# Kernel tuning notes

Measured on AMD Instinct MI355X. Metric: run time of the kernel, lower is better.

## Reference

```python
import jax, jax.numpy as jnp
import numpy as np

B, S, D, H = 2, 2048, 1024, 16
DK = D // H

def setup_inputs() -> dict:
    key = jax.random.key(0)
    ks = jax.random.split(key, 12)
    scale = 1.0 / np.sqrt(D)
    inp = {
        'q': jax.random.normal(ks[0], (B, S, D), jnp.float32),
        'k': jax.random.normal(ks[1], (B, S, D), jnp.float32),
        'v': jax.random.normal(ks[2], (B, S, D), jnp.float32),
        # causal mask: 1 where attending is allowed (j <= i), 0 for future tokens
        'mask': jnp.tril(jnp.ones((S, S), jnp.int32))[None, None, :, :],
        'wq': jax.random.normal(ks[3], (D, D), jnp.float32) * scale,
        'bq': jnp.zeros((D,), jnp.float32),
        'wk': jax.random.normal(ks[4], (D, D), jnp.float32) * scale,
        'bk': jnp.zeros((D,), jnp.float32),
        'wv': jax.random.normal(ks[5], (D, D), jnp.float32) * scale,
        'bv': jnp.zeros((D,), jnp.float32),
        'wo': jax.random.normal(ks[6], (D, D), jnp.float32) * scale,
        'bo': jnp.zeros((D,), jnp.float32),
    }
    return inp


def reference(q, k, v, mask, wq, bq, wk, bk, wv, bv, wo, bo):
    def split_heads(x):
        # [B,S,D] -> [B,H,S,DK]
        return x.reshape(B, S, H, DK).transpose(0, 2, 1, 3)

    query = split_heads(q @ wq + bq)
    key_ = split_heads(k @ wk + bk)
    value = split_heads(v @ wv + bv)

    # [B,H,S,S] attention scores
    scores = jnp.einsum('bhqd,bhkd->bhqk', query, key_) / jnp.sqrt(
        jnp.asarray(DK, jnp.float32))
    scores = jnp.where(mask == 0, jnp.asarray(-1e9, scores.dtype), scores)
    attn = jax.nn.softmax(scores, axis=-1)  # dropout p=0.0 (eval mode)

    x = jnp.einsum('bhqk,bhkd->bhqd', attn, value)  # [B,H,S,DK]
    x = x.transpose(0, 2, 1, 3).reshape(B, S, D)
    return x @ wo + bo
```

## Files before the change

kernel.cpp:

```cpp
#include <hip/hip_runtime.h>
#include <hip/hip_bf16.h>

#define BATCH 2
#define SEQ   2048
#define DMODEL 1024
#define NHEAD 16
#define DK    64
#define MTOK  (BATCH * SEQ)

typedef __attribute__((ext_vector_type(8))) short bf16x8;
typedef __attribute__((ext_vector_type(4))) float f32x4;

__device__ __forceinline__ unsigned short f2bf(float x) {
    unsigned u = __float_as_uint(x);
    u = (u + 0x7FFFu + ((u >> 16) & 1u)) >> 16;
    return (unsigned short)u;
}

__device__ __forceinline__ void store_out(float* p, float v)          { *p = v; }
__device__ __forceinline__ void store_out(unsigned short* p, float v) { *p = f2bf(v); }

__device__ __forceinline__ void g2lds16(const void* g, void* l) {
    __builtin_amdgcn_global_load_lds(
        (const __attribute__((address_space(1))) void*)g,
        (__attribute__((address_space(3))) void*)l, 16, 0, 0);
}

__global__ __launch_bounds__(256) void cvt3_bf16_kernel(
    const float* __restrict__ s0, const float* __restrict__ s1,
    const float* __restrict__ s2,
    unsigned short* __restrict__ d0, unsigned short* __restrict__ d1,
    unsigned short* __restrict__ d2, int n)
{
    const float* src; unsigned short* dst;
    switch (blockIdx.z) {
        case 0:  src = s0; dst = d0; break;
        case 1:  src = s1; dst = d1; break;
        default: src = s2; dst = d2; break;
    }
    int i = (blockIdx.x * 256 + threadIdx.x) * 8;
    if (i >= n) return;
    float4 a = *(const float4*)(src + i);
    float4 b = *(const float4*)(src + i + 4);
    union { unsigned short s[8]; uint4 u; } o;
    o.s[0] = f2bf(a.x); o.s[1] = f2bf(a.y); o.s[2] = f2bf(a.z); o.s[3] = f2bf(a.w);
    o.s[4] = f2bf(b.x); o.s[5] = f2bf(b.y); o.s[6] = f2bf(b.z); o.s[7] = f2bf(b.w);
    *(uint4*)(dst + i) = o.u;
}

__global__ __launch_bounds__(256) void wtrans_kernel(
    const float* __restrict__ w0, const float* __restrict__ w1,
    const float* __restrict__ w2, const float* __restrict__ w3,
    unsigned short* __restrict__ t0, unsigned short* __restrict__ t1,
    unsigned short* __restrict__ t2, unsigned short* __restrict__ t3)
{
    __shared__ float tile[32][33];
    const float* W; unsigned short* T;
    switch (blockIdx.z) {
        case 0:  W = w0; T = t0; break;
        case 1:  W = w1; T = t1; break;
        case 2:  W = w2; T = t2; break;
        default: W = w3; T = t3; break;
    }
    const int n0 = blockIdx.x * 32, k0 = blockIdx.y * 32;
    const int t  = threadIdx.x;
    const int r  = t >> 3;
    const int c4 = (t & 7) * 4;

    float4 v = *(const float4*)&W[(size_t)(k0 + r) * DMODEL + n0 + c4];
    tile[r][c4 + 0] = v.x; tile[r][c4 + 1] = v.y;
    tile[r][c4 + 2] = v.z; tile[r][c4 + 3] = v.w;
    __syncthreads();

    union { unsigned short s[4]; uint2 u; } o;
#pragma unroll
    for (int u = 0; u < 4; ++u) o.s[u] = f2bf(tile[c4 + u][r]);
    *(uint2*)&T[(size_t)(n0 + r) * DMODEL + k0 + c4] = o.u;
}

struct GemmP {
    const unsigned short* A;
    const unsigned short* Bt;
    const float* bias;
    void* C;
    int N, K, ctShift, biasByRow;
    float scale;
};
struct Gemm3 { GemmP p[3]; };

template <typename OutT, int NTILE>
__global__ __launch_bounds__(256) void gemm_lds_kernel(Gemm3 g)
{
    __shared__ unsigned short sA[16 * 512];
    __shared__ unsigned short sB[4 * NTILE * 512];

    const GemmP p = g.p[blockIdx.z];
    const unsigned short* __restrict__ A  = p.A;
    const unsigned short* __restrict__ Bt = p.Bt;
    OutT* __restrict__ C = (OutT*)p.C;
    const int K = p.K, N = p.N;

    const int bid = blockIdx.x;
    const int bx = bid & ((1 << p.ctShift) - 1);
    const int by = bid >> p.ctShift;
    const int row0 = by * 128;
    const int col0 = bx * (NTILE * 32);

    const int t    = threadIdx.x;
    const int w    = t >> 6;
    const int lane = t & 63;
    const int ln   = lane & 15;
    const int qg   = lane >> 4;
    const int wm   = w >> 1;
    const int wn   = w & 1;

    const int PW = 4 + NTILE;
    const unsigned short* sp[PW];
    unsigned short* lp[PW];
#pragma unroll
    for (int i = 0; i < PW; ++i) {
        const int s = w * PW + i;
        if (s < 16) {
            const int mtg = s >> 1, kc = s & 1;
            sp[i] = A + (size_t)(row0 + mtg * 16 + ln) * K + kc * 32 + qg * 8;
            lp[i] = &sA[s * 512];
        } else {
            const int bi = s - 16;
            const int ntg = bi >> 1, kc = bi & 1;
            sp[i] = Bt + (size_t)(col0 + ntg * 16 + ln) * K + kc * 32 + qg * 8;
            lp[i] = &sB[bi * 512];
        }
    }

    f32x4 acc[4][NTILE];
#pragma unroll
    for (int mt = 0; mt < 4; ++mt)
#pragma unroll
        for (int nt = 0; nt < NTILE; ++nt) acc[mt][nt] = (f32x4){0.f, 0.f, 0.f, 0.f};

    for (int kt = 0; kt < K / 64; ++kt) {
        __syncthreads();
        const int koff = kt * 64;
#pragma unroll
        for (int i = 0; i < PW; ++i)
            g2lds16(sp[i] + koff, lp[i]);
        __syncthreads();

#pragma unroll
        for (int kc = 0; kc < 2; ++kc) {
            bf16x8 aF[4], bF[NTILE];
#pragma unroll
            for (int mt = 0; mt < 4; ++mt)
                aF[mt] = *(const bf16x8*)&sA[(((wm * 4 + mt) * 2) + kc) * 512 + lane * 8];
#pragma unroll
            for (int nt = 0; nt < NTILE; ++nt)
                bF[nt] = *(const bf16x8*)&sB[(((wn * NTILE + nt) * 2) + kc) * 512 + lane * 8];
#pragma unroll
            for (int mt = 0; mt < 4; ++mt)
#pragma unroll
                for (int nt = 0; nt < NTILE; ++nt)
                    acc[mt][nt] = __builtin_amdgcn_mfma_f32_16x16x32_bf16(
                        aF[mt], bF[nt], acc[mt][nt], 0, 0, 0);
        }
    }

    float bcol[NTILE], brow[4][4];
    if (!p.biasByRow) {
#pragma unroll
        for (int nt = 0; nt < NTILE; ++nt)
            bcol[nt] = p.bias[col0 + wn * NTILE * 16 + nt * 16 + ln];
    } else {
#pragma unroll
        for (int mt = 0; mt < 4; ++mt)
#pragma unroll
            for (int r = 0; r < 4; ++r)
                brow[mt][r] = p.bias[row0 + wm * 64 + mt * 16 + qg * 4 + r];
    }

#pragma unroll
    for (int mt = 0; mt < 4; ++mt)
#pragma unroll
        for (int nt = 0; nt < NTILE; ++nt)
#pragma unroll
            for (int r = 0; r < 4; ++r) {
                int row = row0 + wm * 64 + mt * 16 + qg * 4 + r;
                int col = col0 + wn * NTILE * 16 + nt * 16 + ln;
                float bb = p.biasByRow ? brow[mt][r] : bcol[nt];
                store_out(&C[(size_t)row * N + col], (acc[mt][nt][r] + bb) * p.scale);
            }
}

#define BR 64
#define BC 64
#define PSTR 72

__global__ __launch_bounds__(256) void attn_mfma_kernel(
    const unsigned short* __restrict__ Qg, const unsigned short* __restrict__ Kg,
    const unsigned short* __restrict__ VT, unsigned short* __restrict__ O)
{
    __shared__ unsigned short sK[2][8 * 512];
    __shared__ unsigned short sV[2][8 * 512];
    __shared__ unsigned short sQ[8 * 512];
    __shared__ unsigned short sP[BR * PSTR];

    const int t    = threadIdx.x;
    const int w    = t >> 6;
    const int lane = t & 63;
    const int ln   = lane & 15;
    const int qg   = lane >> 4;

    const int id  = blockIdx.x;
    const int bh  = id & 31;
    const int qt  = (SEQ / BR - 1) - (id >> 5);
    const int b   = bh >> 4;
    const int h   = bh & 15;
    const int qi0 = qt * BR;

    const size_t rowbase = (size_t)b * SEQ;
    const size_t colbase = (size_t)h * DK;

#pragma unroll
    for (int i = 0; i < 2; ++i) {
        const int s = w * 2 + i;
        const int nt = s >> 1, kc = s & 1;
        g2lds16(Qg + (rowbase + qi0 + w * 16 + ln) * DMODEL + colbase + i * 32 + qg * 8,
                &sQ[s * 512]);
        g2lds16(Kg + (rowbase + nt * 16 + ln) * DMODEL + colbase + kc * 32 + qg * 8,
                &sK[0][s * 512]);
        g2lds16(VT + (size_t)(colbase + nt * 16 + ln) * MTOK + rowbase + kc * 32 + qg * 8,
                &sV[0][s * 512]);
    }
    __syncthreads();

    bf16x8 aq[2];
#pragma unroll
    for (int kc = 0; kc < 2; ++kc)
        aq[kc] = *(const bf16x8*)&sQ[(w * 2 + kc) * 512 + lane * 8];

    const short one_bf = (short)0x3F80;
    const bf16x8 bone = (bf16x8){one_bf, one_bf, one_bf, one_bf,
                                 one_bf, one_bf, one_bf, one_bf};

    f32x4 ofrag[4];
#pragma unroll
    for (int nt = 0; nt < 4; ++nt) ofrag[nt] = (f32x4){0.f, 0.f, 0.f, 0.f};
    f32x4 osum = (f32x4){0.f, 0.f, 0.f, 0.f};
    float m_r[4];
#pragma unroll
    for (int r = 0; r < 4; ++r) m_r[r] = -3.0e38f;

    const int ntiles = qt + 1;
    for (int jt = 0; jt < ntiles; ++jt) {
        const int cur = jt & 1;

        if (jt + 1 < ntiles) {
            const int j1 = (jt + 1) * BC;
            const int nb = cur ^ 1;
#pragma unroll
            for (int i = 0; i < 2; ++i) {
                const int s = w * 2 + i;
                const int nt = s >> 1, kc = s & 1;
                g2lds16(Kg + (rowbase + j1 + nt * 16 + ln) * DMODEL + colbase + kc * 32 + qg * 8,
                        &sK[nb][s * 512]);
                g2lds16(VT + (size_t)(colbase + nt * 16 + ln) * MTOK + rowbase + j1 + kc * 32 + qg * 8,
                        &sV[nb][s * 512]);
            }
        }

        f32x4 sf[4];
#pragma unroll
        for (int nt = 0; nt < 4; ++nt) {
            f32x4 a2 = (f32x4){0.f, 0.f, 0.f, 0.f};
#pragma unroll
            for (int kc = 0; kc < 2; ++kc) {
                bf16x8 bk = *(const bf16x8*)&sK[cur][(nt * 2 + kc) * 512 + lane * 8];
                a2 = __builtin_amdgcn_mfma_f32_16x16x32_bf16(aq[kc], bk, a2, 0, 0, 0);
            }
            sf[nt] = a2;
        }

        if (jt == ntiles - 1) {
#pragma unroll
            for (int nt = 0; nt < 4; ++nt)
#pragma unroll
                for (int r = 0; r < 4; ++r) {
                    int qrow = w * 16 + qg * 4 + r;
                    int col  = nt * 16 + ln;
                    if (col > qrow) sf[nt][r] = -1.0e30f;
                }
        }

        float rmax[4];
#pragma unroll
        for (int r = 0; r < 4; ++r)
            rmax[r] = fmaxf(fmaxf(sf[0][r], sf[1][r]), fmaxf(sf[2][r], sf[3][r]));
#pragma unroll
        for (int off = 8; off >= 1; off >>= 1)
#pragma unroll
            for (int r = 0; r < 4; ++r)
                rmax[r] = fmaxf(rmax[r], __shfl_xor(rmax[r], off));

        float alpha[4];
#pragma unroll
        for (int r = 0; r < 4; ++r) {
            float mn = fmaxf(m_r[r], rmax[r]);
            alpha[r] = exp2f(m_r[r] - mn);
            m_r[r] = mn;
        }

#pragma unroll
        for (int nt = 0; nt < 4; ++nt)
#pragma unroll
            for (int r = 0; r < 4; ++r) {
                float pv = exp2f(sf[nt][r] - m_r[r]);
                int row = w * 16 + qg * 4 + r;
                int col = (nt * 16 + ln) ^ (((w * 4 + qg) & 7) * 8);
                sP[row * PSTR + col] = f2bf(pv);
            }

#pragma unroll
        for (int nt = 0; nt < 4; ++nt)
#pragma unroll
            for (int r = 0; r < 4; ++r) ofrag[nt][r] *= alpha[r];
#pragma unroll
        for (int r = 0; r < 4; ++r) osum[r] *= alpha[r];

        bf16x8 apf[2];
#pragma unroll
        for (int kc = 0; kc < 2; ++kc) {
            int row = w * 16 + ln;
            int col = (kc * 32 + qg * 8) ^ ((((row >> 2) & 7)) * 8);
            apf[kc] = *(const bf16x8*)&sP[row * PSTR + col];
        }

#pragma unroll
        for (int kc = 0; kc < 2; ++kc)
            osum = __builtin_amdgcn_mfma_f32_16x16x32_bf16(apf[kc], bone, osum, 0, 0, 0);
#pragma unroll
        for (int nt = 0; nt < 4; ++nt) {
#pragma unroll
            for (int kc = 0; kc < 2; ++kc) {
                bf16x8 bv = *(const bf16x8*)&sV[cur][(nt * 2 + kc) * 512 + lane * 8];
                ofrag[nt] = __builtin_amdgcn_mfma_f32_16x16x32_bf16(apf[kc], bv, ofrag[nt], 0, 0, 0);
            }
        }

        __syncthreads();
    }

    float inv[4];
#pragma unroll
    for (int r = 0; r < 4; ++r) inv[r] = 1.0f / osum[r];
#pragma unroll
    for (int nt = 0; nt < 4; ++nt)
#pragma unroll
        for (int r = 0; r < 4; ++r) {
            int gq = qi0 + w * 16 + qg * 4 + r;
            O[(rowbase + gq) * DMODEL + colbase + nt * 16 + ln] =
                f2bf(ofrag[nt][r] * inv[r]);
        }
}

extern "C" void kernel_launch(void* const* d_in, const int* in_sizes, int n_in,
                              void* d_out, int out_size, void* d_ws, size_t ws_size,
                              hipStream_t stream)
{
    const float* q  = (const float*)d_in[0];
    const float* k  = (const float*)d_in[1];
    const float* v  = (const float*)d_in[2];
    const float* wq = (const float*)d_in[4];
    const float* bq = (const float*)d_in[5];
    const float* wk = (const float*)d_in[6];
    const float* bk = (const float*)d_in[7];
    const float* wv = (const float*)d_in[8];
    const float* bv = (const float*)d_in[9];
    const float* wo = (const float*)d_in[10];
    const float* bo = (const float*)d_in[11];
    float* out = (float*)d_out;

    const size_t mat  = (size_t)MTOK * DMODEL;
    const size_t wmat = (size_t)DMODEL * DMODEL;
    unsigned short* Abq = (unsigned short*)d_ws;
    unsigned short* Abk = Abq + mat;
    unsigned short* Abv = Abk + mat;
    unsigned short* WtQ = Abv + mat;
    unsigned short* WtK = WtQ + wmat;
    unsigned short* WtV = WtK + wmat;
    unsigned short* WtO = WtV + wmat;
    unsigned short* Qb  = WtO + wmat;
    unsigned short* Kb  = Qb + mat;
    unsigned short* VT  = Kb + mat;
    unsigned short* CTX = VT + mat;

    cvt3_bf16_kernel<<<dim3((unsigned)(mat / 2048), 1, 3), 256, 0, stream>>>(
        q, k, v, Abq, Abk, Abv, (int)mat);
    wtrans_kernel<<<dim3(32, 32, 4), 256, 0, stream>>>(wq, wk, wv, wo, WtQ, WtK, WtV, WtO);

    const float qscale = 0.125f * 1.44269504088896f;
    Gemm3 g;
    g.p[0] = (GemmP){Abq, WtQ, bq, (void*)Qb, DMODEL, DMODEL, 3, 0, qscale};
    g.p[1] = (GemmP){Abk, WtK, bk, (void*)Kb, DMODEL, DMODEL, 3, 0, 1.0f};
    g.p[2] = (GemmP){WtV, Abv, bv, (void*)VT, MTOK,   DMODEL, 5, 1, 1.0f};
    gemm_lds_kernel<unsigned short, 4><<<dim3(256, 1, 3), 256, 0, stream>>>(g);

    attn_mfma_kernel<<<BATCH * NHEAD * (SEQ / BR), 256, 0, stream>>>(Qb, Kb, VT, CTX);

    Gemm3 go;
    go.p[0] = (GemmP){CTX, WtO, bo, (void*)out, DMODEL, DMODEL, 4, 0, 1.0f};
    go.p[1] = go.p[0];
    go.p[2] = go.p[0];
    gemm_lds_kernel<float, 2><<<dim3(512, 1, 1), 256, 0, stream>>>(go);
}
```

Baseline: 272.6 us.

## Fuse fp32-to-bf16 activation conversion into GEMM and process two query tiles per attention block

Drops the separate activation conversion kernel: the projection GEMM now loads fp32 A or B tiles straight into LDS and packs them to bf16 when reading fragments. This removes a full write and re-read of the three activation matrices, at the cost of twice the LDS footprint and extra conversion work in the GEMM inner loop. The attention kernel now gives each block two 64-row query tiles, so each K/V tile is reused across both, and it halves the grid with a 2-blocks-per-CU launch bound. The added accumulator state may raise register pressure.

```diff
diff --git a/kernel.cpp b/kernel.cpp
--- a/kernel.cpp
+++ b/kernel.cpp
@@ -26,26 +26,13 @@
         (__attribute__((address_space(3))) void*)l, 16, 0, 0);
 }
 
-__global__ __launch_bounds__(256) void cvt3_bf16_kernel(
-    const float* __restrict__ s0, const float* __restrict__ s1,
-    const float* __restrict__ s2,
-    unsigned short* __restrict__ d0, unsigned short* __restrict__ d1,
-    unsigned short* __restrict__ d2, int n)
-{
-    const float* src; unsigned short* dst;
-    switch (blockIdx.z) {
-        case 0:  src = s0; dst = d0; break;
-        case 1:  src = s1; dst = d1; break;
-        default: src = s2; dst = d2; break;
-    }
-    int i = (blockIdx.x * 256 + threadIdx.x) * 8;
-    if (i >= n) return;
-    float4 a = *(const float4*)(src + i);
-    float4 b = *(const float4*)(src + i + 4);
-    union { unsigned short s[8]; uint4 u; } o;
-    o.s[0] = f2bf(a.x); o.s[1] = f2bf(a.y); o.s[2] = f2bf(a.z); o.s[3] = f2bf(a.w);
-    o.s[4] = f2bf(b.x); o.s[5] = f2bf(b.y); o.s[6] = f2bf(b.z); o.s[7] = f2bf(b.w);
-    *(uint4*)(dst + i) = o.u;
+__device__ __forceinline__ bf16x8 pack8(f32x4 lo, f32x4 hi) {
+    union { bf16x8 v; __hip_bfloat162 h[4]; } u;
+    u.h[0] = __float22bfloat162_rn(float2{lo[0], lo[1]});
+    u.h[1] = __float22bfloat162_rn(float2{lo[2], lo[3]});
+    u.h[2] = __float22bfloat162_rn(float2{hi[0], hi[1]});
+    u.h[3] = __float22bfloat162_rn(float2{hi[2], hi[3]});
+    return u.v;
 }
 
 __global__ __launch_bounds__(256) void wtrans_kernel(
@@ -79,26 +66,24 @@
 }
 
 struct GemmP {
-    const unsigned short* A;
-    const unsigned short* Bt;
+    const void* A;
+    const void* Bt;
     const float* bias;
     void* C;
-    int N, K, ctShift, biasByRow;
+    int N, K, ctShift, biasByRow, aF32, bF32;
     float scale;
 };
 struct Gemm3 { GemmP p[3]; };
 
-template <typename OutT, int NTILE>
+template <typename OutT, int NTILE, int TOTB>
 __global__ __launch_bounds__(256) void gemm_lds_kernel(Gemm3 g)
 {
-    __shared__ unsigned short sA[16 * 512];
-    __shared__ unsigned short sB[4 * NTILE * 512];
+    __shared__ unsigned char smem[TOTB * 1024];
 
     const GemmP p = g.p[blockIdx.z];
-    const unsigned short* __restrict__ A  = p.A;
-    const unsigned short* __restrict__ Bt = p.Bt;
     OutT* __restrict__ C = (OutT*)p.C;
     const int K = p.K, N = p.N;
+    const int nA = p.aF32 ? 32 : 16;
 
     const int bid = blockIdx.x;
     const int bx = bid & ((1 << p.ctShift) - 1);
@@ -114,23 +99,40 @@
     const int wm   = w >> 1;
     const int wn   = w & 1;
 
-    const int PW = 4 + NTILE;
-    const unsigned short* sp[PW];
-    unsigned short* lp[PW];
+    const int PW = TOTB / 4;
+    const unsigned char* sp[PW];
+    int bstep[PW];
 #pragma unroll
     for (int i = 0; i < PW; ++i) {
         const int s = w * PW + i;
-        if (s < 16) {
-            const int mtg = s >> 1, kc = s & 1;
-            sp[i] = A + (size_t)(row0 + mtg * 16 + ln) * K + kc * 32 + qg * 8;
-            lp[i] = &sA[s * 512];
+        if (s < nA) {
+            if (p.aF32) {
+                const int mtg = s >> 2, kc = (s >> 1) & 1, half = s & 1;
+                sp[i] = (const unsigned char*)p.A +
+                        ((size_t)(row0 + mtg * 16 + ln) * K + kc * 32 + qg * 8 + half * 4) * 4;
+                bstep[i] = 256;
+            } else {
+                const int mtg = s >> 1, kc = s & 1;
+                sp[i] = (const unsigned char*)p.A +
+                        ((size_t)(row0 + mtg * 16 + ln) * K + kc * 32 + qg * 8) * 2;
+                bstep[i] = 128;
+            }
         } else {
-            const int bi = s - 16;
-            const int ntg = bi >> 1, kc = bi & 1;
-            sp[i] = Bt + (size_t)(col0 + ntg * 16 + ln) * K + kc * 32 + qg * 8;
-            lp[i] = &sB[bi * 512];
-        }
-    }
+            const int bi = s - nA;
+            if (p.bF32) {
+                const int ntg = bi >> 2, kc = (bi >> 1) & 1, half = bi & 1;
+                sp[i] = (const unsigned char*)p.Bt +
+                        ((size_t)(col0 + ntg * 16 + ln) * K + kc * 32 + qg * 8 + half * 4) * 4;
+                bstep[i] = 256;
+            } else {
+                const int ntg = bi >> 1, kc = bi & 1;
+                sp[i] = (const unsigned char*)p.Bt +
+                        ((size_t)(col0 + ntg * 16 + ln) * K + kc * 32 + qg * 8) * 2;
+                bstep[i] = 128;
+            }
+        }
+    }
+    unsigned char* const sB = smem + nA * 1024;
 
     f32x4 acc[4][NTILE];
 #pragma unroll
@@ -140,21 +142,38 @@
 
     for (int kt = 0; kt < K / 64; ++kt) {
         __syncthreads();
-        const int koff = kt * 64;
-#pragma unroll
-        for (int i = 0; i < PW; ++i)
-            g2lds16(sp[i] + koff, lp[i]);
+#pragma unroll
+        for (int i = 0; i < PW; ++i) {
+            g2lds16(sp[i], smem + (w * PW + i) * 1024);
+            sp[i] += bstep[i];
+        }
         __syncthreads();
 
 #pragma unroll
         for (int kc = 0; kc < 2; ++kc) {
             bf16x8 aF[4], bF[NTILE];
 #pragma unroll
-            for (int mt = 0; mt < 4; ++mt)
-                aF[mt] = *(const bf16x8*)&sA[(((wm * 4 + mt) * 2) + kc) * 512 + lane * 8];
-#pragma unroll
-            for (int nt = 0; nt < NTILE; ++nt)
-                bF[nt] = *(const bf16x8*)&sB[(((wn * NTILE + nt) * 2) + kc) * 512 + lane * 8];
+            for (int mt = 0; mt < 4; ++mt) {
+                const int fb = ((wm * 4 + mt) * 2) + kc;
+                if (p.aF32) {
+                    f32x4 lo = *(const f32x4*)(smem + (fb * 2 + 0) * 1024 + lane * 16);
+                    f32x4 hi = *(const f32x4*)(smem + (fb * 2 + 1) * 1024 + lane * 16);
+                    aF[mt] = pack8(lo, hi);
+                } else {
+                    aF[mt] = *(const bf16x8*)(smem + fb * 1024 + lane * 16);
+                }
+            }
+#pragma unroll
+            for (int nt = 0; nt < NTILE; ++nt) {
+                const int fb = ((wn * NTILE + nt) * 2) + kc;
+                if (p.bF32) {
+                    f32x4 lo = *(const f32x4*)(sB + (fb * 2 + 0) * 1024 + lane * 16);
+                    f32x4 hi = *(const f32x4*)(sB + (fb * 2 + 1) * 1024 + lane * 16);
+                    bF[nt] = pack8(lo, hi);
+                } else {
+                    bF[nt] = *(const bf16x8*)(sB + fb * 1024 + lane * 16);
+                }
+            }
 #pragma unroll
             for (int mt = 0; mt < 4; ++mt)
 #pragma unroll
@@ -190,18 +209,16 @@
             }
 }
 
-#define BR 64
-#define BC 64
 #define PSTR 72
 
-__global__ __launch_bounds__(256) void attn_mfma_kernel(
+__global__ __launch_bounds__(256, 2) void attn_mfma_kernel(
     const unsigned short* __restrict__ Qg, const unsigned short* __restrict__ Kg,
     const unsigned short* __restrict__ VT, unsigned short* __restrict__ O)
 {
+    __shared__ unsigned short sQ[16 * 512];
     __shared__ unsigned short sK[2][8 * 512];
     __shared__ unsigned short sV[2][8 * 512];
-    __shared__ unsigned short sQ[8 * 512];
-    __shared__ unsigned short sP[BR * PSTR];
+    __shared__ unsigned short sP[64 * PSTR];
 
     const int t    = threadIdx.x;
     const int w    = t >> 6;
@@ -211,20 +228,27 @@
 
     const int id  = blockIdx.x;
     const int bh  = id & 31;
-    const int qt  = (SEQ / BR - 1) - (id >> 5);
+    const int Pp  = 15 - (id >> 5);
     const int b   = bh >> 4;
     const int h   = bh & 15;
-    const int qi0 = qt * BR;
+    const int qbase = Pp * 128;
 
     const size_t rowbase = (size_t)b * SEQ;
     const size_t colbase = (size_t)h * DK;
 
+#pragma unroll
+    for (int st = 0; st < 2; ++st)
+#pragma unroll
+        for (int i = 0; i < 2; ++i) {
+            const int sidx = (st * 4 + w) * 2 + i;
+            g2lds16(Qg + (rowbase + qbase + st * 64 + w * 16 + ln) * DMODEL
+                        + colbase + i * 32 + qg * 8,
+                    &sQ[sidx * 512]);
+        }
 #pragma unroll
     for (int i = 0; i < 2; ++i) {
         const int s = w * 2 + i;
         const int nt = s >> 1, kc = s & 1;
-        g2lds16(Qg + (rowbase + qi0 + w * 16 + ln) * DMODEL + colbase + i * 32 + qg * 8,
-                &sQ[s * 512]);
         g2lds16(Kg + (rowbase + nt * 16 + ln) * DMODEL + colbase + kc * 32 + qg * 8,
                 &sK[0][s * 512]);
         g2lds16(VT + (size_t)(colbase + nt * 16 + ln) * MTOK + rowbase + kc * 32 + qg * 8,
@@ -232,29 +256,35 @@
     }
     __syncthreads();
 
-    bf16x8 aq[2];
-#pragma unroll
-    for (int kc = 0; kc < 2; ++kc)
-        aq[kc] = *(const bf16x8*)&sQ[(w * 2 + kc) * 512 + lane * 8];
+    bf16x8 aq[2][2];
+#pragma unroll
+    for (int st = 0; st < 2; ++st)
+#pragma unroll
+        for (int kc = 0; kc < 2; ++kc)
+            aq[st][kc] = *(const bf16x8*)&sQ[((st * 4 + w) * 2 + kc) * 512 + lane * 8];
 
     const short one_bf = (short)0x3F80;
     const bf16x8 bone = (bf16x8){one_bf, one_bf, one_bf, one_bf,
                                  one_bf, one_bf, one_bf, one_bf};
 
-    f32x4 ofrag[4];
-#pragma unroll
-    for (int nt = 0; nt < 4; ++nt) ofrag[nt] = (f32x4){0.f, 0.f, 0.f, 0.f};
-    f32x4 osum = (f32x4){0.f, 0.f, 0.f, 0.f};
-    float m_r[4];
-#pragma unroll
-    for (int r = 0; r < 4; ++r) m_r[r] = -3.0e38f;
-
-    const int ntiles = qt + 1;
+    f32x4 ofrag[2][4];
+    f32x4 osum[2];
+    float m_r[2][4];
+#pragma unroll
+    for (int st = 0; st < 2; ++st) {
+#pragma unroll
+        for (int nt = 0; nt < 4; ++nt) ofrag[st][nt] = (f32x4){0.f, 0.f, 0.f, 0.f};
+        osum[st] = (f32x4){0.f, 0.f, 0.f, 0.f};
+#pragma unroll
+        for (int r = 0; r < 4; ++r) m_r[st][r] = -3.0e38f;
+    }
+
+    const int ntiles = 2 * Pp + 2;
     for (int jt = 0; jt < ntiles; ++jt) {
         const int cur = jt & 1;
 
         if (jt + 1 < ntiles) {
-            const int j1 = (jt + 1) * BC;
+            const int j1 = (jt + 1) * 64;
             const int nb = cur ^ 1;
 #pragma unroll
             for (int i = 0; i < 2; ++i) {
@@ -267,98 +297,104 @@
             }
         }
 
-        f32x4 sf[4];
-#pragma unroll
-        for (int nt = 0; nt < 4; ++nt) {
-            f32x4 a2 = (f32x4){0.f, 0.f, 0.f, 0.f};
+#pragma unroll
+        for (int st = 0; st < 2; ++st) {
+            f32x4 sf[4];
+#pragma unroll
+            for (int nt = 0; nt < 4; ++nt) {
+                f32x4 a2 = (f32x4){0.f, 0.f, 0.f, 0.f};
+#pragma unroll
+                for (int kc = 0; kc < 2; ++kc) {
+                    bf16x8 bk = *(const bf16x8*)&sK[cur][(nt * 2 + kc) * 512 + lane * 8];
+                    a2 = __builtin_amdgcn_mfma_f32_16x16x32_bf16(aq[st][kc], bk, a2, 0, 0, 0);
+                }
+                sf[nt] = a2;
+            }
+
+            if (jt >= 2 * Pp + st) {
+#pragma unroll
+                for (int nt = 0; nt < 4; ++nt)
+#pragma unroll
+                    for (int r = 0; r < 4; ++r) {
+                        int grow = qbase + st * 64 + w * 16 + qg * 4 + r;
+                        int gcol = jt * 64 + nt * 16 + ln;
+                        if (gcol > grow) sf[nt][r] = -1.0e30f;
+                    }
+            }
+
+            float rmax[4];
+#pragma unroll
+            for (int r = 0; r < 4; ++r)
+                rmax[r] = fmaxf(fmaxf(sf[0][r], sf[1][r]), fmaxf(sf[2][r], sf[3][r]));
+#pragma unroll
+            for (int off = 8; off >= 1; off >>= 1)
+#pragma unroll
+                for (int r = 0; r < 4; ++r)
+                    rmax[r] = fmaxf(rmax[r], __shfl_xor(rmax[r], off));
+
+            float alpha[4];
+#pragma unroll
+            for (int r = 0; r < 4; ++r) {
+                float mn = fmaxf(m_r[st][r], rmax[r]);
+                alpha[r] = exp2f(m_r[st][r] - mn);
+                m_r[st][r] = mn;
+            }
+
+#pragma unroll
+            for (int nt = 0; nt < 4; ++nt)
+#pragma unroll
+                for (int r = 0; r < 4; ++r) {
+                    float pv = exp2f(sf[nt][r] - m_r[st][r]);
+                    int row = w * 16 + qg * 4 + r;
+                    int col = (nt * 16 + ln) ^ (((w * 4 + qg) & 7) * 8);
+                    sP[row * PSTR + col] = f2bf(pv);
+                }
+
+#pragma unroll
+            for (int nt = 0; nt < 4; ++nt)
+#pragma unroll
+                for (int r = 0; r < 4; ++r) ofrag[st][nt][r] *= alpha[r];
+#pragma unroll
+            for (int r = 0; r < 4; ++r) osum[st][r] *= alpha[r];
+
+            bf16x8 apf[2];
 #pragma unroll
             for (int kc = 0; kc < 2; ++kc) {
-                bf16x8 bk = *(const bf16x8*)&sK[cur][(nt * 2 + kc) * 512 + lane * 8];
-                a2 = __builtin_amdgcn_mfma_f32_16x16x32_bf16(aq[kc], bk, a2, 0, 0, 0);
-            }
-            sf[nt] = a2;
-        }
-
-        if (jt == ntiles - 1) {
+                int row = w * 16 + ln;
+                int col = (kc * 32 + qg * 8) ^ ((((row >> 2) & 7)) * 8);
+                apf[kc] = *(const bf16x8*)&sP[row * PSTR + col];
+            }
+
+#pragma unroll
+            for (int kc = 0; kc < 2; ++kc)
+                osum[st] = __builtin_amdgcn_mfma_f32_16x16x32_bf16(apf[kc], bone, osum[st], 0, 0, 0);
 #pragma unroll
             for (int nt = 0; nt < 4; ++nt)
 #pragma unroll
-                for (int r = 0; r < 4; ++r) {
-                    int qrow = w * 16 + qg * 4 + r;
-                    int col  = nt * 16 + ln;
-                    if (col > qrow) sf[nt][r] = -1.0e30f;
+                for (int kc = 0; kc < 2; ++kc) {
+                    bf16x8 bv = *(const bf16x8*)&sV[cur][(nt * 2 + kc) * 512 + lane * 8];
+                    ofrag[st][nt] = __builtin_amdgcn_mfma_f32_16x16x32_bf16(
+                        apf[kc], bv, ofrag[st][nt], 0, 0, 0);
                 }
         }
 
-        float rmax[4];
-#pragma unroll
-        for (int r = 0; r < 4; ++r)
-            rmax[r] = fmaxf(fmaxf(sf[0][r], sf[1][r]), fmaxf(sf[2][r], sf[3][r]));
-#pragma unroll
-        for (int off = 8; off >= 1; off >>= 1)
-#pragma unroll
-            for (int r = 0; r < 4; ++r)
-                rmax[r] = fmaxf(rmax[r], __shfl_xor(rmax[r], off));
-
-        float alpha[4];
-#pragma unroll
-        for (int r = 0; r < 4; ++r) {
-            float mn = fmaxf(m_r[r], rmax[r]);
-            alpha[r] = exp2f(m_r[r] - mn);
-            m_r[r] = mn;
-        }
-
+        __syncthreads();
+    }
+
+#pragma unroll
+    for (int st = 0; st < 2; ++st) {
+        float inv[4];
+#pragma unroll
+        for (int r = 0; r < 4; ++r) inv[r] = 1.0f / osum[st][r];
 #pragma unroll
         for (int nt = 0; nt < 4; ++nt)
 #pragma unroll
             for (int r = 0; r < 4; ++r) {
-                float pv = exp2f(sf[nt][r] - m_r[r]);
-                int row = w * 16 + qg * 4 + r;
-                int col = (nt * 16 + ln) ^ (((w * 4 + qg) & 7) * 8);
-                sP[row * PSTR + col] = f2bf(pv);
-            }
-
-#pragma unroll
-        for (int nt = 0; nt < 4; ++nt)
-#pragma unroll
-            for (int r = 0; r < 4; ++r) ofrag[nt][r] *= alpha[r];
-#pragma unroll
-        for (int r = 0; r < 4; ++r) osum[r] *= alpha[r];
-
-        bf16x8 apf[2];
-#pragma unroll
-        for (int kc = 0; kc < 2; ++kc) {
-            int row = w * 16 + ln;
-            int col = (kc * 32 + qg * 8) ^ ((((row >> 2) & 7)) * 8);
-            apf[kc] = *(const bf16x8*)&sP[row * PSTR + col];
-        }
-
-#pragma unroll
-        for (int kc = 0; kc < 2; ++kc)
-            osum = __builtin_amdgcn_mfma_f32_16x16x32_bf16(apf[kc], bone, osum, 0, 0, 0);
-#pragma unroll
-        for (int nt = 0; nt < 4; ++nt) {
-#pragma unroll
-            for (int kc = 0; kc < 2; ++kc) {
-                bf16x8 bv = *(const bf16x8*)&sV[cur][(nt * 2 + kc) * 512 + lane * 8];
-                ofrag[nt] = __builtin_amdgcn_mfma_f32_16x16x32_bf16(apf[kc], bv, ofrag[nt], 0, 0, 0);
-            }
-        }
-
-        __syncthreads();
-    }
-
-    float inv[4];
-#pragma unroll
-    for (int r = 0; r < 4; ++r) inv[r] = 1.0f / osum[r];
-#pragma unroll
-    for (int nt = 0; nt < 4; ++nt)
-#pragma unroll
-        for (int r = 0; r < 4; ++r) {
-            int gq = qi0 + w * 16 + qg * 4 + r;
-            O[(rowbase + gq) * DMODEL + colbase + nt * 16 + ln] =
-                f2bf(ofrag[nt][r] * inv[r]);
-        }
+                int gq = qbase + st * 64 + w * 16 + qg * 4 + r;
+                O[(rowbase + gq) * DMODEL + colbase + nt * 16 + ln] =
+                    f2bf(ofrag[st][nt][r] * inv[r]);
+            }
+    }
 }
 
 extern "C" void kernel_launch(void* const* d_in, const int* in_sizes, int n_in,
@@ -380,10 +416,7 @@
 
     const size_t mat  = (size_t)MTOK * DMODEL;
     const size_t wmat = (size_t)DMODEL * DMODEL;
-    unsigned short* Abq = (unsigned short*)d_ws;
-    unsigned short* Abk = Abq + mat;
-    unsigned short* Abv = Abk + mat;
-    unsigned short* WtQ = Abv + mat;
+    unsigned short* WtQ = (unsigned short*)d_ws;
     unsigned short* WtK = WtQ + wmat;
     unsigned short* WtV = WtK + wmat;
     unsigned short* WtO = WtV + wmat;
@@ -392,22 +425,20 @@
     unsigned short* VT  = Kb + mat;
     unsigned short* CTX = VT + mat;
 
-    cvt3_bf16_kernel<<<dim3((unsigned)(mat / 2048), 1, 3), 256, 0, stream>>>(
-        q, k, v, Abq, Abk, Abv, (int)mat);
     wtrans_kernel<<<dim3(32, 32, 4), 256, 0, stream>>>(wq, wk, wv, wo, WtQ, WtK, WtV, WtO);
 
     const float qscale = 0.125f * 1.44269504088896f;
     Gemm3 g;
-    g.p[0] = (GemmP){Abq, WtQ, bq, (void*)Qb, DMODEL, DMODEL, 3, 0, qscale};
-    g.p[1] = (GemmP){Abk, WtK, bk, (void*)Kb, DMODEL, DMODEL, 3, 0, 1.0f};
-    g.p[2] = (GemmP){WtV, Abv, bv, (void*)VT, MTOK,   DMODEL, 5, 1, 1.0f};
-    gemm_lds_kernel<unsigned short, 4><<<dim3(256, 1, 3), 256, 0, stream>>>(g);
-
-    attn_mfma_kernel<<<BATCH * NHEAD * (SEQ / BR), 256, 0, stream>>>(Qb, Kb, VT, CTX);
+    g.p[0] = (GemmP){q,   WtQ, bq, (void*)Qb, DMODEL, DMODEL, 3, 0, 1, 0, qscale};
+    g.p[1] = (GemmP){k,   WtK, bk, (void*)Kb, DMODEL, DMODEL, 3, 0, 1, 0, 1.0f};
+    g.p[2] = (GemmP){WtV, v,   bv, (void*)VT, MTOK,   DMODEL, 5, 1, 0, 1, 1.0f};
+    gemm_lds_kernel<unsigned short, 4, 48><<<dim3(256, 1, 3), 256, 0, stream>>>(g);
+
+    attn_mfma_kernel<<<512, 256, 0, stream>>>(Qb, Kb, VT, CTX);
 
     Gemm3 go;
-    go.p[0] = (GemmP){CTX, WtO, bo, (void*)out, DMODEL, DMODEL, 4, 0, 1.0f};
+    go.p[0] = (GemmP){CTX, WtO, bo, (void*)out, DMODEL, DMODEL, 4, 0, 0, 0, 1.0f};
     go.p[1] = go.p[0];
     go.p[2] = go.p[0];
-    gemm_lds_kernel<float, 2><<<dim3(512, 1, 1), 256, 0, stream>>>(go);
-}
+    gemm_lds_kernel<float, 2, 24><<<dim3(512, 1, 1), 256, 0, stream>>>(go);
+}
```

New measurement: 322.9 us. +18.4%, slower.
